# Kernel tuning notes

Measured on AMD Instinct MI355X. Metric: run time of the kernel, lower is better.

## Reference

```python
import jax, jax.numpy as jnp
import numpy as np

D_MODEL = 1024
N_HEADS = 16
N_LAYERS = 4
N_LEVELS = 8
B, T = 2, 1024
EPS = 1e-5
ADALN_K = 0.1
ADALN_C = 2.0
FMAX = float(np.finfo(np.float32).max)


def setup_inputs() -> dict:
    key = jax.random.key(0)
    ks = jax.random.split(key, 12)
    d, L = D_MODEL, N_LAYERS
    x = jax.random.normal(ks[0], (B, T, d), dtype=jnp.float32)
    # ragged lengths -> padding mask (1 valid, 0 pad), shape (b, t, 1)
    lengths = jnp.array([T, (3 * T) // 4], dtype=jnp.int32)
    m = (jnp.arange(T)[None, :] < lengths[:, None]).astype(jnp.float32)[..., None]
    l = jax.random.randint(ks[1], (B,), 0, N_LEVELS, dtype=jnp.int32)
    s = 0.02
    Wqkv = jax.random.normal(ks[2], (L, d, 3 * d), dtype=jnp.float32) * s
    Wout = jax.random.normal(ks[3], (L, d, d), dtype=jnp.float32) * s
    bout = jnp.zeros((L, d), dtype=jnp.float32)
    adaln_attn = jax.random.normal(ks[4], (L, N_LEVELS, 2 * d), dtype=jnp.float32) * s
    adaln_ffn = jax.random.normal(ks[5], (L, N_LEVELS, 2 * d), dtype=jnp.float32) * s
    W1 = jax.random.normal(ks[6], (L, d, 4 * d), dtype=jnp.float32) * s
    b1 = jnp.zeros((L, 4 * d), dtype=jnp.float32)
    W2 = jax.random.normal(ks[7], (L, 4 * d, d), dtype=jnp.float32) * s
    b2 = jnp.zeros((L, d), dtype=jnp.float32)
    return dict(x=x, m=m, l=l, Wqkv=Wqkv, Wout=Wout, bout=bout,
                adaln_attn=adaln_attn, adaln_ffn=adaln_ffn,
                W1=W1, b1=b1, W2=W2, b2=b2)


def _adaln(x, emb, l):
    # emb: (n_levels, 2d); l: (b,)
    g = emb[l][:, None, :]                      # (b, 1, 2d)
    loggamma, beta = jnp.split(g, 2, axis=-1)
    mu = jnp.mean(x, axis=-1, keepdims=True)
    var = jnp.mean((x - mu) ** 2, axis=-1, keepdims=True)
    h = (x - mu) * jax.lax.rsqrt(var + EPS)
    h = ADALN_C * (1.0 - jax.lax.stop_gradient(ADALN_K * h)) * h
    return jnp.exp(loggamma) * h + beta


def _attention(x, m, Wqkv, Wout, bout):
    b, t, d = x.shape
    h = N_HEADS
    dh = d // h
    qkv = x @ Wqkv                               # (b, t, 3d)
    q, k, v = jnp.split(qkv, 3, axis=-1)
    q = q.reshape(b, t, h, dh)
    k = k.reshape(b, t, h, dh)
    v = v.reshape(b, t, h, dh)
    e = jnp.einsum('bihd,bjhd->bijh', q, k) * (dh ** -0.5)
    kpm = m[:, None, :, :] * m[:, :, None, :]    # (b, i, j, 1)
    causal = jnp.tril(jnp.ones((t, t), dtype=kpm.dtype))[None, :, :, None]
    kpm = kpm * causal
    e = jnp.where(kpm == 0, -FMAX, e)
    a = jax.nn.softmax(e, axis=2)                # softmax over j (dim=2), matches custom softmax
    o = jnp.einsum('bijh,bjhd->bihd', a, v).reshape(b, t, d)
    o = o @ Wout + bout
    return o * m


def reference(x, m, l, Wqkv, Wout, bout, adaln_attn, adaln_ffn, W1, b1, W2, b2):
    for i in range(N_LAYERS):
        # attention sub-block (PrenormResidual with AdaLN, requires_mask=True)
        h = _adaln(x, adaln_attn[i], l) * m
        x = (x + _attention(h, m, Wqkv[i], Wout[i], bout[i])) * m
        # FFN sub-block
        h = _adaln(x, adaln_ffn[i], l) * m
        ff = jax.nn.gelu(h @ W1[i] + b1[i], approximate=False) @ W2[i] + b2[i]
        x = (x + ff) * m
    return x
```

## Files before the change

kernel.cpp:

```cpp
#include <hip/hip_runtime.h>

#define D_MODEL 1024
#define N_HEADS 16
#define DH 64
#define N_LAYERS 4
#define N_LEVELS 8
#define BB 2
#define TT 1024
#define MM (BB*TT)
#define EPSV 1e-5f

typedef float f32x4 __attribute__((ext_vector_type(4)));
typedef short bf16x8 __attribute__((ext_vector_type(8)));
typedef unsigned short u16x4 __attribute__((ext_vector_type(4)));

__device__ __forceinline__ float bf2f(unsigned short u) {
    union { unsigned int i; float f; } c; c.i = ((unsigned int)u) << 16; return c.f;
}
__device__ __forceinline__ unsigned short f2bf(float f) {
    union { float f; unsigned int i; } c; c.f = f;
    unsigned int x = c.i;
    return (unsigned short)((x + 0x7fffu + ((x >> 16) & 1u)) >> 16);
}
__device__ __forceinline__ float cvt_in(const void* src, long long j, int isbf) {
    return isbf ? bf2f(((const unsigned short*)src)[j]) : ((const float*)src)[j];
}

__device__ __forceinline__ void gl_lds16(const unsigned short* g, unsigned short* l) {
    __builtin_amdgcn_global_load_lds(
        (const __attribute__((address_space(1))) unsigned int*)g,
        (__attribute__((address_space(3))) unsigned int*)l,
        16, 0, 0);
}

__global__ void detect_kernel(const unsigned short* __restrict__ x, int* __restrict__ flag) {
    __shared__ int cnts[256];
    int cnt = 0;
    for (int i = threadIdx.x; i < 16384; i += 256) {
        unsigned short u = x[2 * i];
        int e = (u >> 7) & 0xFF;
        if (e >= 110 && e <= 140) cnt++;
    }
    cnts[threadIdx.x] = cnt;
    __syncthreads();
    for (int s = 128; s; s >>= 1) {
        if (threadIdx.x < s) cnts[threadIdx.x] += cnts[threadIdx.x + s];
        __syncthreads();
    }
    if (threadIdx.x == 0) flag[0] = (cnts[0] > 12000) ? 1 : 0;
}

__global__ void load_f32_kernel(const void* __restrict__ src, float* __restrict__ dst,
                                const int* __restrict__ flag, int n) {
    int i = blockIdx.x * 256 + threadIdx.x;
    if (i >= n) return;
    dst[i] = cvt_in(src, i, flag[0]);
}
__global__ void load_small_kernel(const void* m_in, const void* aa, const void* af_,
                                  const void* bo, const void* b1, const void* b2,
                                  float* mf, float* embA, float* embF,
                                  float* boutf, float* b1f, float* b2f,
                                  const int* __restrict__ flag) {
    int i = blockIdx.x * 256 + threadIdx.x;
    int isbf = flag[0];
    if (i < 2048)        mf[i] = cvt_in(m_in, i, isbf);
    else if (i < 67584)  embA[i - 2048] = cvt_in(aa, i - 2048, isbf);
    else if (i < 133120) embF[i - 67584] = cvt_in(af_, i - 67584, isbf);
    else if (i < 137216) boutf[i - 133120] = cvt_in(bo, i - 133120, isbf);
    else if (i < 153600) b1f[i - 137216] = cvt_in(b1, i - 137216, isbf);
    else if (i < 157696) b2f[i - 153600] = cvt_in(b2, i - 153600, isbf);
}

__global__ __launch_bounds__(256)
void transpose_layer_kernel(const void* Wqkv, const void* Wo, const void* W1, const void* W2,
                            unsigned short* wq, unsigned short* wo,
                            unsigned short* w1, unsigned short* w2,
                            const int* __restrict__ flag,
                            long long o_qkv, long long o_o, long long o_1, long long o_2) {
    __shared__ float tile[32][33];
    int bid = blockIdx.x;
    const void* src; unsigned short* dst; long long off; int N, K, nt, kt;
    if (bid < 3072)      { int t = bid;        src = Wqkv; dst = wq; off = o_qkv; N = 3072; K = 1024; nt = t % 96;  kt = t / 96; }
    else if (bid < 4096) { int t = bid - 3072; src = Wo;   dst = wo; off = o_o;   N = 1024; K = 1024; nt = t % 32;  kt = t / 32; }
    else if (bid < 8192) { int t = bid - 4096; src = W1;   dst = w1; off = o_1;   N = 4096; K = 1024; nt = t % 128; kt = t / 128; }
    else                 { int t = bid - 8192; src = W2;   dst = w2; off = o_2;   N = 1024; K = 4096; nt = t % 32;  kt = t / 32; }
    int n0 = nt * 32, k0 = kt * 32;
    int r = threadIdx.x >> 5, c = threadIdx.x & 31;
    int isbf = flag[0];
    #pragma unroll
    for (int rr = 0; rr < 4; ++rr) {
        int k = k0 + r + rr * 8;
        tile[r + rr * 8][c] = cvt_in(src, off + (long long)k * N + n0 + c, isbf);
    }
    __syncthreads();
    #pragma unroll
    for (int rr = 0; rr < 4; ++rr) {
        int n = n0 + r + rr * 8;
        dst[(size_t)n * K + k0 + c] = f2bf(tile[c][r + rr * 8]);
    }
}

__device__ __forceinline__ void blk_sum2_256(float& a, float& b, float* red) {
    #pragma unroll
    for (int off = 32; off; off >>= 1) {
        a += __shfl_down(a, off, 64);
        b += __shfl_down(b, off, 64);
    }
    int tid = threadIdx.x;
    __syncthreads();
    if ((tid & 63) == 0) { red[tid >> 6] = a; red[4 + (tid >> 6)] = b; }
    __syncthreads();
    a = red[0] + red[1] + red[2] + red[3];
    b = red[4] + red[5] + red[6] + red[7];
}

__global__ __launch_bounds__(256)
void adaln_kernel(const float* __restrict__ x,
                  const float* __restrict__ emb,
                  const int* __restrict__ lvl,
                  const float* __restrict__ mvec,
                  unsigned short* __restrict__ h) {
    __shared__ float red[8];
    int row = blockIdx.x;
    int b = row / TT;
    int tid = threadIdx.x;
    const float* xr = x + (size_t)row * D_MODEL;
    float mval = mvec[row];
    unsigned short* hr = h + (size_t)row * D_MODEL;

    if (mval == 0.0f) {
        u16x4 z = (u16x4)0;
        *(u16x4*)(hr + 4 * tid) = z;
        return;
    }

    f32x4 xv = *(const f32x4*)(xr + 4 * tid);
    float s = xv[0] + xv[1] + xv[2] + xv[3];
    float ss = xv[0]*xv[0] + xv[1]*xv[1] + xv[2]*xv[2] + xv[3]*xv[3];
    blk_sum2_256(s, ss, red);
    float mu = s * (1.0f / D_MODEL);
    float var = ss * (1.0f / D_MODEL) - mu * mu;
    float rstd = rsqrtf(var + EPSV);

    int lv = lvl[b];
    const float* g = emb + (size_t)lv * (2 * D_MODEL);
    f32x4 lg = *(const f32x4*)(g + 4 * tid);
    f32x4 lb = *(const f32x4*)(g + D_MODEL + 4 * tid);
    u16x4 r;
    #pragma unroll
    for (int c = 0; c < 4; ++c) {
        float hn = (xv[c] - mu) * rstd;
        float h2 = 2.0f * (1.0f - 0.1f * hn) * hn;
        float o = __expf(lg[c]) * h2 + lb[c];
        r[c] = f2bf(o * mval);
    }
    *(u16x4*)(hr + 4 * tid) = r;
}

#define EPI_STORE 0
#define EPI_GELU  1
#define EPI_RESID 2
#define EPI_PART  3

template<int MI, int NI, int WR, int WC>
__global__ __launch_bounds__(WR * WC * 64)
void gemm8_kernel(const unsigned short* __restrict__ A, int lda,
                  const unsigned short* __restrict__ BT, int ldb,
                  const float* __restrict__ bias,
                  unsigned short* __restrict__ outb,
                  const float* __restrict__ xin,
                  float* __restrict__ xout,
                  const float* __restrict__ mvec,
                  float* __restrict__ pbuf,
                  int M, int N, int K, int mode) {
    constexpr int BM = WR * MI * 16;
    constexpr int BN = WC * NI * 16;
    constexpr int NW = WR * WC;
    __shared__ __align__(16) unsigned short As[2][BM * 32];
    __shared__ __align__(16) unsigned short Bs[2][BN * 32];
    __shared__ int alive;
    int tid = threadIdx.x;
    int wave = tid >> 6;
    int lane = tid & 63;
    int quad = lane >> 4;
    int l16  = lane & 15;
    int tileM = blockIdx.y * BM;
    int tileN = blockIdx.x * BN;
    int wm = (wave % WR) * MI * 16;
    int wn = (wave / WR) * NI * 16;

    if (tid == 0) alive = 0;
    __syncthreads();
    if (tid < BM && mvec[tileM + tid] != 0.0f) alive = 1;
    __syncthreads();

    f32x4 acc[MI][NI] = {};

    if (alive) {
        long long zoff = (long long)blockIdx.z * K;
        const unsigned short* Ab = A  + zoff + (size_t)(tileM + (lane >> 2)) * lda + (lane & 3) * 8;
        const unsigned short* Bb = BT + zoff + (size_t)(tileN + (lane >> 2)) * ldb + (lane & 3) * 8;

        for (int st = wave; st < BM / 16; st += NW)
            gl_lds16(Ab + (size_t)st * 16 * lda, &As[0][st * 512]);
        for (int st = wave; st < BN / 16; st += NW)
            gl_lds16(Bb + (size_t)st * 16 * ldb, &Bs[0][st * 512]);
        __syncthreads();

        int cur = 0;
        for (int k0 = 0; k0 < K; k0 += 32) {
            if (k0 + 32 < K) {
                for (int st = wave; st < BM / 16; st += NW)
                    gl_lds16(Ab + (size_t)st * 16 * lda + k0 + 32, &As[cur ^ 1][st * 512]);
                for (int st = wave; st < BN / 16; st += NW)
                    gl_lds16(Bb + (size_t)st * 16 * ldb + k0 + 32, &Bs[cur ^ 1][st * 512]);
            }

            bf16x8 af[MI], bf[NI];
            #pragma unroll
            for (int mi = 0; mi < MI; ++mi)
                af[mi] = *(const bf16x8*)(&As[cur][(wm + mi * 16 + l16) * 32 + quad * 8]);
            #pragma unroll
            for (int ni = 0; ni < NI; ++ni)
                bf[ni] = *(const bf16x8*)(&Bs[cur][(wn + ni * 16 + l16) * 32 + quad * 8]);
            #pragma unroll
            for (int mi = 0; mi < MI; ++mi)
                #pragma unroll
                for (int ni = 0; ni < NI; ++ni)
                    acc[mi][ni] = __builtin_amdgcn_mfma_f32_16x16x32_bf16(af[mi], bf[ni], acc[mi][ni], 0, 0, 0);

            __syncthreads();
            cur ^= 1;
        }
    }

    #pragma unroll
    for (int mi = 0; mi < MI; ++mi)
    #pragma unroll
    for (int ni = 0; ni < NI; ++ni) {
        #pragma unroll
        for (int r = 0; r < 4; ++r) {
            int row = tileM + wm + mi * 16 + quad * 4 + r;
            int col = tileN + wn + ni * 16 + l16;
            float v = acc[mi][ni][r];
            size_t idx = (size_t)row * N + col;
            if (mode == EPI_STORE) {
                outb[idx] = f2bf(v);
            } else if (mode == EPI_GELU) {
                v += bias[col];
                float gel = 0.5f * v * (1.0f + erff(v * 0.70710678118654752f));
                outb[idx] = f2bf(gel);
            } else if (mode == EPI_RESID) {
                v += bias[col];
                xout[idx] = (xin[idx] + v) * mvec[row];
            } else {
                pbuf[(size_t)blockIdx.z * M * N + idx] = v;
            }
        }
    }
}

#define FA_DPAD 72

__global__ __launch_bounds__(256)
void fattn_split_kernel(const unsigned short* __restrict__ qkv,
                        const float* __restrict__ mvec,
                        float* __restrict__ Opart,
                        float* __restrict__ ml) {
    __shared__ __align__(16) unsigned short Qs[64 * FA_DPAD];
    __shared__ __align__(16) unsigned short Ks[64 * FA_DPAD];
    __shared__ __align__(16) unsigned short Vs[64 * FA_DPAD];
    __shared__ __align__(16) unsigned short Ps[64 * FA_DPAD];
    __shared__ int alive_s;

    int qt  = blockIdx.x;
    int hd  = blockIdx.y;
    int b   = blockIdx.z >> 1;
    int s   = blockIdx.z & 1;
    int tid = threadIdx.x;
    int wave = tid >> 6;
    int lane = tid & 63;
    int quad = lane >> 4;
    int l16  = lane & 15;

    if (tid == 0) alive_s = 0;
    __syncthreads();
    if (tid < 64 && mvec[(size_t)b * TT + qt * 64 + tid] != 0.0f) alive_s = 1;
    __syncthreads();
    bool alive = alive_s != 0;

    const unsigned short* base = qkv + (size_t)b * TT * 3072;

    f32x4 Oacc[4] = {};
    float mstate[4], lstate[4];
    #pragma unroll
    for (int r = 0; r < 4; ++r) {
        mstate[r] = alive ? -1e30f : 0.f;
        lstate[r] = alive ? 0.f : 1.f;
    }

    if (alive) {
        {
            int r = tid >> 2, c = (tid & 3) * 16;
            const unsigned short* src = base + (size_t)(qt * 64 + r) * 3072 + hd * DH + c;
            *(uint4*)(&Qs[r * FA_DPAD + c])     = *(const uint4*)(src);
            *(uint4*)(&Qs[r * FA_DPAD + c + 8]) = *(const uint4*)(src + 8);
        }
        __syncthreads();

        bf16x8 aq[2];
        #pragma unroll
        for (int cc = 0; cc < 2; ++cc)
            aq[cc] = *(const bf16x8*)(&Qs[(wave * 16 + l16) * FA_DPAD + cc * 32 + quad * 8]);

        for (int jt = s; jt <= qt; jt += 2) {
            __syncthreads();
            {
                int r = tid >> 2, c = (tid & 3) * 16;
                const unsigned short* src = base + (size_t)(jt * 64 + r) * 3072 + 1024 + hd * DH + c;
                *(uint4*)(&Ks[r * FA_DPAD + c])     = *(const uint4*)(src);
                *(uint4*)(&Ks[r * FA_DPAD + c + 8]) = *(const uint4*)(src + 8);
            }
            {
                int j = lane, c = wave * 16;
                const unsigned short* src = base + (size_t)(jt * 64 + j) * 3072 + 2048 + hd * DH + c;
                unsigned short tmp[16];
                *(uint4*)(tmp)     = *(const uint4*)(src);
                *(uint4*)(tmp + 8) = *(const uint4*)(src + 8);
                #pragma unroll
                for (int d = 0; d < 16; ++d) Vs[(c + d) * FA_DPAD + j] = tmp[d];
            }
            __syncthreads();

            f32x4 S[4] = {};
            #pragma unroll
            for (int t = 0; t < 4; ++t)
                #pragma unroll
                for (int cc = 0; cc < 2; ++cc) {
                    bf16x8 bk = *(const bf16x8*)(&Ks[(t * 16 + l16) * FA_DPAD + cc * 32 + quad * 8]);
                    S[t] = __builtin_amdgcn_mfma_f32_16x16x32_bf16(aq[cc], bk, S[t], 0, 0, 0);
                }

            int qrow0 = qt * 64 + wave * 16 + quad * 4;
            bool diag = (jt == qt);
            float mnew[4];
            #pragma unroll
            for (int r = 0; r < 4; ++r) {
                float v = -1e30f;
                #pragma unroll
                for (int t = 0; t < 4; ++t) {
                    float sv = S[t][r] * 0.125f;
                    if (diag) {
                        int j = jt * 64 + t * 16 + l16;
                        if (j > qrow0 + r) sv = -1e30f;
                    }
                    S[t][r] = sv;
                    v = fmaxf(v, sv);
                }
                v = fmaxf(v, __shfl_xor(v, 1, 64));
                v = fmaxf(v, __shfl_xor(v, 2, 64));
                v = fmaxf(v, __shfl_xor(v, 4, 64));
                v = fmaxf(v, __shfl_xor(v, 8, 64));
                mnew[r] = fmaxf(mstate[r], v);
            }

            #pragma unroll
            for (int r = 0; r < 4; ++r) {
                float rs = 0.f;
                #pragma unroll
                for (int t = 0; t < 4; ++t) {
                    float p = __expf(S[t][r] - mnew[r]);
                    rs += p;
                    Ps[(wave * 16 + quad * 4 + r) * FA_DPAD + t * 16 + l16] = f2bf(p);
                }
                rs += __shfl_xor(rs, 1, 64);
                rs += __shfl_xor(rs, 2, 64);
                rs += __shfl_xor(rs, 4, 64);
                rs += __shfl_xor(rs, 8, 64);
                float alpha = __expf(mstate[r] - mnew[r]);
                lstate[r] = alpha * lstate[r] + rs;
                mstate[r] = mnew[r];
                #pragma unroll
                for (int t = 0; t < 4; ++t) Oacc[t][r] *= alpha;
            }

            #pragma unroll
            for (int cc = 0; cc < 2; ++cc) {
                bf16x8 ap = *(const bf16x8*)(&Ps[(wave * 16 + l16) * FA_DPAD + cc * 32 + quad * 8]);
                #pragma unroll
                for (int t = 0; t < 4; ++t) {
                    bf16x8 bv = *(const bf16x8*)(&Vs[(t * 16 + l16) * FA_DPAD + cc * 32 + quad * 8]);
                    Oacc[t] = __builtin_amdgcn_mfma_f32_16x16x32_bf16(ap, bv, Oacc[t], 0, 0, 0);
                }
            }
        }
    }

    #pragma unroll
    for (int r = 0; r < 4; ++r) {
        int qi = qt * 64 + wave * 16 + quad * 4 + r;
        size_t row = (size_t)b * TT + qi;
        float* orow = Opart + (size_t)s * MM * D_MODEL + row * D_MODEL + hd * DH;
        #pragma unroll
        for (int t = 0; t < 4; ++t)
            orow[t * 16 + l16] = Oacc[t][r];
        if (l16 == 0) {
            float* mlp = ml + (((size_t)s * MM + row) * N_HEADS + hd) * 2;
            mlp[0] = mstate[r];
            mlp[1] = lstate[r];
        }
    }
}

__global__ void attn_merge_kernel(const float* __restrict__ Opart,
                                  const float* __restrict__ ml,
                                  unsigned short* __restrict__ ob) {
    int i = blockIdx.x * 256 + threadIdx.x;
    int row = i >> 10;
    int hd  = (i >> 6) & 15;
    const float* ml0 = ml + (((size_t)row) * N_HEADS + hd) * 2;
    const float* ml1 = ml + (((size_t)MM + row) * N_HEADS + hd) * 2;
    float m0 = ml0[0], l0 = ml0[1];
    float m1 = ml1[0], l1 = ml1[1];
    float M = fmaxf(m0, m1);
    float w0 = __expf(m0 - M), w1 = __expf(m1 - M);
    float den = w0 * l0 + w1 * l1;
    float num = w0 * Opart[i] + w1 * Opart[(size_t)MM * D_MODEL + i];
    ob[i] = f2bf(num / den);
}

__global__ void combine2_kernel(float* __restrict__ xf,
                                const float* __restrict__ pbuf,
                                const float* __restrict__ bias,
                                const float* __restrict__ mvec,
                                void* __restrict__ outp,
                                const int* __restrict__ flag, int n) {
    int i = blockIdx.x * 256 + threadIdx.x;
    if (i >= n) return;
    int row = i >> 10, col = i & 1023;
    float v = (xf[i] + pbuf[i] + pbuf[n + i] + bias[col]) * mvec[row];
    xf[i] = v;
    if (outp) {
        if (flag[0]) ((unsigned short*)outp)[i] = f2bf(v);
        else         ((float*)outp)[i] = v;
    }
}

#define MB (1048576u)
#define WS_FLAG   0u
#define WS_MF     4096u
#define WS_EMBA   (WS_MF + 8192u)
#define WS_EMBF   (WS_EMBA + 262144u)
#define WS_BOUT   (WS_EMBF + 262144u)
#define WS_B1     (WS_BOUT + 16384u)
#define WS_B2     (WS_B1 + 65536u)
#define WS_XF     (1u*MB)
#define WS_H      (9u*MB)
#define WS_QKV    (13u*MB)
#define WS_OB     (25u*MB)
#define WS_PART   (9u*MB)
#define WS_ML     (9u*MB)
#define WS_FF1    (29u*MB)
#define WS_OPART  (29u*MB)
#define WS_WQKV   (45u*MB)
#define WS_WOUT   (51u*MB)
#define WS_W1     (53u*MB)
#define WS_W2     (61u*MB)

extern "C" void kernel_launch(void* const* d_in, const int* in_sizes, int n_in,
                              void* d_out, int out_size, void* d_ws, size_t ws_size,
                              hipStream_t stream) {
    const void* x_in  = d_in[0];
    const void* m_in  = d_in[1];
    const int*  l_in  = (const int*)d_in[2];
    const void* Wqkv  = d_in[3];
    const void* Wout  = d_in[4];
    const void* boutp = d_in[5];
    const void* ada_a = d_in[6];
    const void* ada_f = d_in[7];
    const void* W1    = d_in[8];
    const void* b1    = d_in[9];
    const void* W2    = d_in[10];
    const void* b2    = d_in[11];

    char* ws = (char*)d_ws;
    int*            flag = (int*)(ws + WS_FLAG);
    float*          mf   = (float*)(ws + WS_MF);
    float*          embA = (float*)(ws + WS_EMBA);
    float*          embF = (float*)(ws + WS_EMBF);
    float*          boutf= (float*)(ws + WS_BOUT);
    float*          b1f  = (float*)(ws + WS_B1);
    float*          b2f  = (float*)(ws + WS_B2);
    float*          xf   = (float*)(ws + WS_XF);
    unsigned short* h    = (unsigned short*)(ws + WS_H);
    unsigned short* qkv  = (unsigned short*)(ws + WS_QKV);
    unsigned short* ob   = (unsigned short*)(ws + WS_OB);
    float*          part = (float*)(ws + WS_PART);
    float*          mlb  = (float*)(ws + WS_ML);
    float*          opart= (float*)(ws + WS_OPART);
    unsigned short* ff1  = (unsigned short*)(ws + WS_FF1);
    unsigned short* wqkvt= (unsigned short*)(ws + WS_WQKV);
    unsigned short* woutt= (unsigned short*)(ws + WS_WOUT);
    unsigned short* w1t  = (unsigned short*)(ws + WS_W1);
    unsigned short* w2t  = (unsigned short*)(ws + WS_W2);

    const int n = MM * D_MODEL;

    detect_kernel<<<1, 256, 0, stream>>>((const unsigned short*)x_in, flag);
    load_f32_kernel<<<n / 256, 256, 0, stream>>>(x_in, xf, flag, n);
    load_small_kernel<<<(157696 + 255) / 256, 256, 0, stream>>>(
        m_in, ada_a, ada_f, boutp, b1, b2, mf, embA, embF, boutf, b1f, b2f, flag);

    const long long nqkv = (long long)D_MODEL * 3 * D_MODEL;
    const long long nsq  = (long long)D_MODEL * D_MODEL;
    const long long nw1  = (long long)D_MODEL * 4 * D_MODEL;

    for (int i = 0; i < N_LAYERS; ++i) {
        transpose_layer_kernel<<<12288, 256, 0, stream>>>(
            Wqkv, Wout, W1, W2, wqkvt, woutt, w1t, w2t, flag,
            i * nqkv, i * nsq, i * nw1, i * nw1);

        adaln_kernel<<<MM, 256, 0, stream>>>(xf, embA + (size_t)i * N_LEVELS * 2 * D_MODEL, l_in, mf, h);
        gemm8_kernel<4,2,2,2><<<dim3(3072 / 64, MM / 128), 256, 0, stream>>>(
            h, 1024, wqkvt, 1024, nullptr, qkv, nullptr, nullptr, mf, nullptr,
            MM, 3072, 1024, EPI_STORE);
        fattn_split_kernel<<<dim3(TT / 64, N_HEADS, BB * 2), 256, 0, stream>>>(qkv, mf, opart, mlb);
        attn_merge_kernel<<<n / 256, 256, 0, stream>>>(opart, mlb, ob);
        gemm8_kernel<2,2,4,2><<<dim3(1024 / 64, MM / 128), 512, 0, stream>>>(
            ob, 1024, woutt, 1024, boutf + (size_t)i * D_MODEL, nullptr, xf, xf, mf, nullptr,
            MM, 1024, 1024, EPI_RESID);
        adaln_kernel<<<MM, 256, 0, stream>>>(xf, embF + (size_t)i * N_LEVELS * 2 * D_MODEL, l_in, mf, h);
        gemm8_kernel<4,2,2,4><<<dim3(4096 / 128, MM / 128), 512, 0, stream>>>(
            h, 1024, w1t, 1024, b1f + (size_t)i * 4 * D_MODEL, ff1, nullptr, nullptr, mf, nullptr,
            MM, 4096, 1024, EPI_GELU);
        gemm8_kernel<2,2,4,2><<<dim3(1024 / 64, MM / 128, 2), 512, 0, stream>>>(
            ff1, 4096, w2t, 4096, nullptr, nullptr, nullptr, nullptr, mf, part,
            MM, 1024, 2048, EPI_PART);
        combine2_kernel<<<n / 256, 256, 0, stream>>>(
            xf, part, b2f + (size_t)i * D_MODEL, mf,
            (i == N_LAYERS - 1) ? d_out : nullptr, flag, n);
    }
}
```

Baseline: 972.1 us.

## Deepen GEMM K-loop pipeline to four LDS buffers with vmcnt waits

After: 938.8 us. -3.4%, faster.

```diff
diff --git a/kernel.cpp b/kernel.cpp
--- a/kernel.cpp
+++ b/kernel.cpp
@@ -31,6 +31,10 @@
         (const __attribute__((address_space(1))) unsigned int*)g,
         (__attribute__((address_space(3))) unsigned int*)l,
         16, 0, 0);
+}
+
+template<int N> __device__ __forceinline__ void wait_vm() {
+    asm volatile("s_waitcnt vmcnt(%0)" :: "i"(N) : "memory");
 }
 
 __global__ void detect_kernel(const unsigned short* __restrict__ x, int* __restrict__ flag) {
@@ -176,8 +180,14 @@
     constexpr int BM = WR * MI * 16;
     constexpr int BN = WC * NI * 16;
     constexpr int NW = WR * WC;
-    __shared__ __align__(16) unsigned short As[2][BM * 32];
-    __shared__ __align__(16) unsigned short Bs[2][BN * 32];
+    constexpr int NSA = BM / 16;
+    constexpr int NSB = BN / 16;
+    static_assert(NSA % NW == 0, "A staging must divide evenly over waves");
+    constexpr int LA  = NSA / NW;
+    constexpr int LB0 = NSB / NW;
+    constexpr int LBr = NSB % NW;
+    __shared__ __align__(16) unsigned short As[4][BM * 32];
+    __shared__ __align__(16) unsigned short Bs[4][BN * 32];
     __shared__ int alive;
     int tid = threadIdx.x;
     int wave = tid >> 6;
@@ -201,36 +211,50 @@
         const unsigned short* Ab = A  + zoff + (size_t)(tileM + (lane >> 2)) * lda + (lane & 3) * 8;
         const unsigned short* Bb = BT + zoff + (size_t)(tileN + (lane >> 2)) * ldb + (lane & 3) * 8;
 
-        for (int st = wave; st < BM / 16; st += NW)
-            gl_lds16(Ab + (size_t)st * 16 * lda, &As[0][st * 512]);
-        for (int st = wave; st < BN / 16; st += NW)
-            gl_lds16(Bb + (size_t)st * 16 * ldb, &Bs[0][st * 512]);
-        __syncthreads();
-
-        int cur = 0;
-        for (int k0 = 0; k0 < K; k0 += 32) {
-            if (k0 + 32 < K) {
-                for (int st = wave; st < BM / 16; st += NW)
-                    gl_lds16(Ab + (size_t)st * 16 * lda + k0 + 32, &As[cur ^ 1][st * 512]);
-                for (int st = wave; st < BN / 16; st += NW)
-                    gl_lds16(Bb + (size_t)st * 16 * ldb + k0 + 32, &Bs[cur ^ 1][st * 512]);
-            }
-
+        auto stage = [&](int t, int buf) {
+            int k0 = t * 32;
+            #pragma unroll
+            for (int st = wave, i = 0; i < LA; st += NW, ++i)
+                gl_lds16(Ab + (size_t)st * 16 * lda + k0, &As[buf][st * 512]);
+            for (int st = wave; st < NSB; st += NW)
+                gl_lds16(Bb + (size_t)st * 16 * ldb + k0, &Bs[buf][st * 512]);
+        };
+        auto compute = [&](int buf) {
+            __builtin_amdgcn_sched_barrier(0);
             bf16x8 af[MI], bf[NI];
             #pragma unroll
             for (int mi = 0; mi < MI; ++mi)
-                af[mi] = *(const bf16x8*)(&As[cur][(wm + mi * 16 + l16) * 32 + quad * 8]);
+                af[mi] = *(const bf16x8*)(&As[buf][(wm + mi * 16 + l16) * 32 + quad * 8]);
             #pragma unroll
             for (int ni = 0; ni < NI; ++ni)
-                bf[ni] = *(const bf16x8*)(&Bs[cur][(wn + ni * 16 + l16) * 32 + quad * 8]);
+                bf[ni] = *(const bf16x8*)(&Bs[buf][(wn + ni * 16 + l16) * 32 + quad * 8]);
             #pragma unroll
             for (int mi = 0; mi < MI; ++mi)
                 #pragma unroll
                 for (int ni = 0; ni < NI; ++ni)
                     acc[mi][ni] = __builtin_amdgcn_mfma_f32_16x16x32_bf16(af[mi], bf[ni], acc[mi][ni], 0, 0, 0);
-
-            __syncthreads();
-            cur ^= 1;
+        };
+
+        int nt = K / 32;
+        stage(0, 0);
+        stage(1, 1);
+        for (int t = 0; t + 2 < nt; ++t) {
+            stage(t + 2, (t + 2) & 3);
+            if (LBr && wave < LBr) wait_vm<2 * (LA + LB0 + 1)>();
+            else                   wait_vm<2 * (LA + LB0)>();
+            __builtin_amdgcn_s_barrier();
+            compute(t & 3);
+        }
+        {
+            if (LBr && wave < LBr) wait_vm<LA + LB0 + 1>();
+            else                   wait_vm<LA + LB0>();
+            __builtin_amdgcn_s_barrier();
+            compute((nt - 2) & 3);
+        }
+        {
+            wait_vm<0>();
+            __builtin_amdgcn_s_barrier();
+            compute((nt - 1) & 3);
         }
     }
 
```
